# Optimization experiments

Measured on AMD Instinct MI355X. Metric: run time of the kernel, lower is better.

## Reference

```python
import math
import jax, jax.numpy as jnp
import numpy as np

B, S, D = 1, 2048, 4096
H, KV, Dh = 32, 8, 128          # query heads, kv heads, head dim
G = H // KV                      # GQA group size
THETA = 10000.0
FACTOR = 4.0
BETA_FAST, BETA_SLOW, ORIG_MAX = 32, 1, 32768


def _yarn_rope_cache(seq_len):
    """YaRN-scaled RoPE cos/sin cache, matching YaRNRotaryEmbedding._build_cache."""
    inv_freq = 1.0 / (THETA ** (np.arange(0, Dh, 2, dtype=np.float32) / Dh))
    low = ORIG_MAX / (2 * math.pi * BETA_SLOW)
    high = ORIG_MAX / (2 * math.pi * BETA_FAST)
    freq = 1.0 / inv_freq
    smooth = np.clip((freq - low) / (high - low), 0.0, 1.0)
    inv_freq = (1.0 - smooth) * inv_freq + smooth * (inv_freq / FACTOR)
    t = np.arange(seq_len, dtype=np.float32)
    freqs = np.outer(t, inv_freq)                 # [S, Dh/2]
    emb = np.concatenate([freqs, freqs], axis=-1) # [S, Dh]
    return np.cos(emb).astype(np.float32), np.sin(emb).astype(np.float32)


def _rotate_half(x):
    x1, x2 = jnp.split(x, 2, axis=-1)
    return jnp.concatenate([-x2, x1], axis=-1)


def setup_inputs() -> dict:
    key = jax.random.key(0)
    k0, k1, k2, k3, k4 = jax.random.split(key, 5)
    scale = 0.02
    hidden_states = jax.random.normal(k0, (B, S, D), jnp.float32)
    Wq = jax.random.normal(k1, (H * Dh, D), jnp.float32) * scale
    Wk = jax.random.normal(k2, (KV * Dh, D), jnp.float32) * scale
    Wv = jax.random.normal(k3, (KV * Dh, D), jnp.float32) * scale
    Wo = jax.random.normal(k4, (D, H * Dh), jnp.float32) * scale
    cos_np, sin_np = _yarn_rope_cache(S)
    return {"hidden_states": hidden_states, "Wq": Wq, "Wk": Wk, "Wv": Wv,
            "Wo": Wo, "cos": jnp.asarray(cos_np), "sin": jnp.asarray(sin_np)}


def reference(hidden_states, Wq, Wk, Wv, Wo, cos, sin):
    x = hidden_states
    b, s, _ = x.shape
    # QKV projections (Linear, no bias): y = x @ W.T
    q = jnp.einsum('bsd,ed->bse', x, Wq).reshape(b, s, H, Dh).transpose(0, 2, 1, 3)   # [B,H,S,Dh]
    k = jnp.einsum('bsd,ed->bse', x, Wk).reshape(b, s, KV, Dh).transpose(0, 2, 1, 3)  # [B,KV,S,Dh]
    v = jnp.einsum('bsd,ed->bse', x, Wv).reshape(b, s, KV, Dh).transpose(0, 2, 1, 3)  # [B,KV,S,Dh]
    # YaRN RoPE (cos/sin: [S,Dh], broadcast over batch/head)
    c = cos[None, None, :, :]
    sn = sin[None, None, :, :]
    q = q * c + _rotate_half(q) * sn
    k = k * c + _rotate_half(k) * sn
    # GQA: group query heads over kv heads instead of materializing repeat_interleave
    qg = q.reshape(b, KV, G, s, Dh)
    scores = jnp.einsum('bkgqd,bknd->bkgqn', qg, k) / math.sqrt(Dh)  # [B,KV,G,S,S]
    causal = jnp.tril(jnp.ones((s, s), dtype=bool))
    scores = jnp.where(causal[None, None, None], scores, jnp.finfo(scores.dtype).min)
    w = jax.nn.softmax(scores.astype(jnp.float32), axis=-1).astype(x.dtype)
    attn = jnp.einsum('bkgqn,bknd->bkgqd', w, v)                      # [B,KV,G,S,Dh]
    attn = attn.reshape(b, H, s, Dh).transpose(0, 2, 1, 3).reshape(b, s, H * Dh)
    return jnp.einsum('bse,de->bsd', attn, Wo)
```

## Files before the change

### kernel.cpp

```cpp
#include <hip/hip_runtime.h>

#define S_LEN 2048
#define DMODEL 4096
#define NH 32
#define NKV 8
#define DH 128
#define QDIM (NH*DH)
#define NQKV 6144
#define SCALE 0.08838834764831845f

typedef __attribute__((ext_vector_type(8))) short short8;
typedef __attribute__((ext_vector_type(4))) float f32x4;
typedef __attribute__((ext_vector_type(4))) unsigned short us4;

__device__ __forceinline__ unsigned short f2bf(float f) {
  union { float f; unsigned int u; } v; v.f = f;
  unsigned int r = v.u + 0x7FFFu + ((v.u >> 16) & 1u);
  return (unsigned short)(r >> 16);
}
__device__ __forceinline__ float bf2f(unsigned short h) {
  union { unsigned int u; float f; } v; v.u = ((unsigned int)h) << 16;
  return v.f;
}

__global__ __launch_bounds__(256) void cvt_all(const float* __restrict__ x,
                                               const float* __restrict__ Wq,
                                               const float* __restrict__ Wk,
                                               const float* __restrict__ Wv,
                                               unsigned short* __restrict__ xb,
                                               unsigned short* __restrict__ Wqkvb) {
  const int blk = blockIdx.x;
  const float* src; unsigned short* dst; int off;
  if (blk < 8192)       { src = x;  dst = xb;               off = blk; }
  else if (blk < 24576) { src = Wq; dst = Wqkvb;            off = blk - 8192; }
  else if (blk < 28672) { src = Wk; dst = Wqkvb + 16777216; off = blk - 24576; }
  else                  { src = Wv; dst = Wqkvb + 20971520; off = blk - 28672; }
  int i = off * 256 + threadIdx.x;
  const float4 f = reinterpret_cast<const float4*>(src)[i];
  us4 o;
  o.x = f2bf(f.x); o.y = f2bf(f.y); o.z = f2bf(f.z); o.w = f2bf(f.w);
  reinterpret_cast<us4*>(dst)[i] = o;
}

template<int M_, int N_, int K_, int BM_, int BN_, int OUT_BF16, int CHN>
__global__ __launch_bounds__(512) void gemm8p(const unsigned short* __restrict__ A,
                                              const unsigned short* __restrict__ B,
                                              void* __restrict__ Cv) {
  constexpr int ATILE = BM_ * 128;
  constexpr int BTILE = BN_ * 128;
  constexpr int BUF = ATILE + BTILE;
  constexpr int LPA = BM_ / 64;
  constexpr int LPB = BN_ / 64;
  constexpr int VM  = LPA + LPB;
  constexpr int MI = BM_ / 32, NF = BN_ / 64;
  constexpr int MIL = MI / 2, NFL = NF / 2;
  constexpr int NT = K_ / 64;
  __shared__ char lds[2 * BUF];

  const int tid = threadIdx.x;
  const int lane = tid & 63, wave = tid >> 6;
  const int wm = wave >> 2, wn = wave & 3;
  const int fr = lane & 15, fq = lane >> 4;

  const int lin = blockIdx.x;
  const int xcd = lin & 7;
  const int slot = lin >> 3;
  const long n0 = (long)(xcd * CHN + slot % CHN) * BN_;
  const long m0 = (long)(slot / CHN) * BM_;

  auto STAGE_A = [&](int t, int c) {
#pragma unroll
    for (int u = 0; u < LPA; ++u) {
      int b = u * 8192 + tid * 16;
      int row = b >> 7;
      int off = (b & 127) ^ ((row & 7) << 4);
      __builtin_amdgcn_global_load_lds(
        (const __attribute__((address_space(1))) void*)((const char*)A + ((m0 + row) * (long)K_ + t * 64) * 2 + off),
        (__attribute__((address_space(3))) void*)(lds + c * BUF + b), 16, 0, 0);
    }
  };
  auto STAGE_B = [&](int t, int c) {
#pragma unroll
    for (int u = 0; u < LPB; ++u) {
      int b = u * 8192 + tid * 16;
      int row = b >> 7;
      int off = (b & 127) ^ ((row & 7) << 4);
      __builtin_amdgcn_global_load_lds(
        (const __attribute__((address_space(1))) void*)((const char*)B + ((n0 + row) * (long)K_ + t * 64) * 2 + off),
        (__attribute__((address_space(3))) void*)(lds + c * BUF + ATILE + b), 16, 0, 0);
    }
  };
#define VMCNT_STEADY() do { if constexpr (VM == 6) asm volatile("s_waitcnt vmcnt(6)" ::: "memory"); \
                            else if constexpr (VM == 7) asm volatile("s_waitcnt vmcnt(7)" ::: "memory"); \
                            else asm volatile("s_waitcnt vmcnt(8)" ::: "memory"); } while (0)

  f32x4 acc[MI][NF] = {};
  short8 af[MI][2];
  short8 bf[NF][2];

  STAGE_A(0, 0); STAGE_B(0, 0);
  STAGE_A(1, 1); STAGE_B(1, 1);
  VMCNT_STEADY();
  __builtin_amdgcn_s_barrier();

  for (int t = 0; t < NT; ++t) {
    const int c = t & 1;
    const char* tb = lds + c * BUF;

#pragma unroll
    for (int mi = 0; mi < MIL; ++mi) {
      int row = wm * (BM_ / 2) + mi * 16 + fr;
#pragma unroll
      for (int ks = 0; ks < 2; ++ks)
        af[mi][ks] = *(const short8*)(tb + row * 128 + ((ks * 64 + fq * 16) ^ ((row & 7) << 4)));
    }
#pragma unroll
    for (int ni = 0; ni < NFL; ++ni) {
      int row = wn * (BN_ / 4) + ni * 16 + fr;
#pragma unroll
      for (int ks = 0; ks < 2; ++ks)
        bf[ni][ks] = *(const short8*)(tb + ATILE + row * 128 + ((ks * 64 + fq * 16) ^ ((row & 7) << 4)));
    }
    __builtin_amdgcn_s_barrier();
    __builtin_amdgcn_s_setprio(1);
#pragma unroll
    for (int mi = 0; mi < MIL; ++mi)
#pragma unroll
      for (int ni = 0; ni < NFL; ++ni)
#pragma unroll
        for (int ks = 0; ks < 2; ++ks)
          acc[mi][ni] = __builtin_amdgcn_mfma_f32_16x16x32_bf16(af[mi][ks], bf[ni][ks], acc[mi][ni], 0, 0, 0);
    __builtin_amdgcn_s_setprio(0);
    __builtin_amdgcn_s_barrier();

#pragma unroll
    for (int mi = MIL; mi < MI; ++mi) {
      int row = wm * (BM_ / 2) + mi * 16 + fr;
#pragma unroll
      for (int ks = 0; ks < 2; ++ks)
        af[mi][ks] = *(const short8*)(tb + row * 128 + ((ks * 64 + fq * 16) ^ ((row & 7) << 4)));
    }
#pragma unroll
    for (int ni = NFL; ni < NF; ++ni) {
      int row = wn * (BN_ / 4) + ni * 16 + fr;
#pragma unroll
      for (int ks = 0; ks < 2; ++ks)
        bf[ni][ks] = *(const short8*)(tb + ATILE + row * 128 + ((ks * 64 + fq * 16) ^ ((row & 7) << 4)));
    }
    __builtin_amdgcn_s_barrier();
    __builtin_amdgcn_s_setprio(1);
#pragma unroll
    for (int mi = 0; mi < MIL; ++mi)
#pragma unroll
      for (int ni = NFL; ni < NF; ++ni)
#pragma unroll
        for (int ks = 0; ks < 2; ++ks)
          acc[mi][ni] = __builtin_amdgcn_mfma_f32_16x16x32_bf16(af[mi][ks], bf[ni][ks], acc[mi][ni], 0, 0, 0);
    __builtin_amdgcn_s_setprio(0);
    __builtin_amdgcn_s_barrier();

    if (t + 2 < NT) STAGE_A(t + 2, c);
    __builtin_amdgcn_s_setprio(1);
#pragma unroll
    for (int mi = MIL; mi < MI; ++mi)
#pragma unroll
      for (int ni = 0; ni < NFL; ++ni)
#pragma unroll
        for (int ks = 0; ks < 2; ++ks)
          acc[mi][ni] = __builtin_amdgcn_mfma_f32_16x16x32_bf16(af[mi][ks], bf[ni][ks], acc[mi][ni], 0, 0, 0);
    __builtin_amdgcn_s_setprio(0);
    __builtin_amdgcn_s_barrier();

    if (t + 2 < NT) STAGE_B(t + 2, c);
    __builtin_amdgcn_s_setprio(1);
#pragma unroll
    for (int mi = MIL; mi < MI; ++mi)
#pragma unroll
      for (int ni = NFL; ni < NF; ++ni)
#pragma unroll
        for (int ks = 0; ks < 2; ++ks)
          acc[mi][ni] = __builtin_amdgcn_mfma_f32_16x16x32_bf16(af[mi][ks], bf[ni][ks], acc[mi][ni], 0, 0, 0);
    __builtin_amdgcn_s_setprio(0);
    if (t + 2 < NT) { VMCNT_STEADY(); }
    else if (t + 1 < NT) { asm volatile("s_waitcnt vmcnt(0)" ::: "memory"); }
    __builtin_amdgcn_s_barrier();
  }
#undef VMCNT_STEADY

#pragma unroll
  for (int mi = 0; mi < MI; ++mi)
#pragma unroll
    for (int ni = 0; ni < NF; ++ni)
#pragma unroll
      for (int j = 0; j < 4; ++j) {
        long r = m0 + wm * (BM_ / 2) + mi * 16 + fq * 4 + j;
        long cc = n0 + wn * (BN_ / 4) + ni * 16 + fr;
        float v = acc[mi][ni][j];
        if (OUT_BF16) ((unsigned short*)Cv)[r * N_ + cc] = f2bf(v);
        else          ((float*)Cv)[r * N_ + cc] = v;
      }
}

template<int M_, int N_, int K_, int BM_, int BN_, int OUT_BF16, int CHN>
__global__ __launch_bounds__(512) void gemm8p3(const unsigned short* __restrict__ A,
                                               const unsigned short* __restrict__ B,
                                               void* __restrict__ Cv) {
  constexpr int ATILE = BM_ * 128;
  constexpr int BTILE = BN_ * 128;
  constexpr int BUF = ATILE + BTILE;
  constexpr int LPA = BM_ / 64;
  constexpr int LPB = BN_ / 64;
  constexpr int MI = BM_ / 32, NF = BN_ / 64;
  constexpr int MIL = MI / 2, NFL = NF / 2;
  constexpr int NT = K_ / 64;
  __shared__ char lds[3 * BUF];

  const int tid = threadIdx.x;
  const int lane = tid & 63, wave = tid >> 6;
  const int wm = wave >> 2, wn = wave & 3;
  const int fr = lane & 15, fq = lane >> 4;

  const int lin = blockIdx.x;
  const int xcd = lin & 7;
  const int slot = lin >> 3;
  const long n0 = (long)(xcd * CHN + slot % CHN) * BN_;
  const long m0 = (long)(slot / CHN) * BM_;

  auto STAGE_A = [&](int t, int c) {
#pragma unroll
    for (int u = 0; u < LPA; ++u) {
      int b = u * 8192 + tid * 16;
      int row = b >> 7;
      int off = (b & 127) ^ ((row & 7) << 4);
      __builtin_amdgcn_global_load_lds(
        (const __attribute__((address_space(1))) void*)((const char*)A + ((m0 + row) * (long)K_ + t * 64) * 2 + off),
        (__attribute__((address_space(3))) void*)(lds + c * BUF + b), 16, 0, 0);
    }
  };
  auto STAGE_B_HALF = [&](int t, int c, int half) {
#pragma unroll
    for (int u = 0; u < LPB / 2; ++u) {
      int b = (half * (LPB / 2) + u) * 8192 + tid * 16;
      int row = b >> 7;
      int off = (b & 127) ^ ((row & 7) << 4);
      __builtin_amdgcn_global_load_lds(
        (const __attribute__((address_space(1))) void*)((const char*)B + ((n0 + row) * (long)K_ + t * 64) * 2 + off),
        (__attribute__((address_space(3))) void*)(lds + c * BUF + ATILE + b), 16, 0, 0);
    }
  };

  f32x4 acc[MI][NF] = {};
  short8 af[MI][2];
  short8 bf[NF][2];

  STAGE_A(0, 0); STAGE_B_HALF(0, 0, 0); STAGE_B_HALF(0, 0, 1);
  STAGE_A(1, 1); STAGE_B_HALF(1, 1, 0); STAGE_B_HALF(1, 1, 1);
  asm volatile("s_waitcnt vmcnt(0)" ::: "memory");
  __builtin_amdgcn_s_barrier();

  for (int t = 0; t < NT; ++t) {
    const char* tb = lds + (t % 3) * BUF;
    const int c2 = (t + 2) % 3;

#pragma unroll
    for (int mi = 0; mi < MIL; ++mi) {
      int row = wm * (BM_ / 2) + mi * 16 + fr;
#pragma unroll
      for (int ks = 0; ks < 2; ++ks)
        af[mi][ks] = *(const short8*)(tb + row * 128 + ((ks * 64 + fq * 16) ^ ((row & 7) << 4)));
    }
#pragma unroll
    for (int ni = 0; ni < NFL; ++ni) {
      int row = wn * (BN_ / 4) + ni * 16 + fr;
#pragma unroll
      for (int ks = 0; ks < 2; ++ks)
        bf[ni][ks] = *(const short8*)(tb + ATILE + row * 128 + ((ks * 64 + fq * 16) ^ ((row & 7) << 4)));
    }
    if (t + 2 < NT) STAGE_A(t + 2, c2);
    __builtin_amdgcn_s_barrier();
    __builtin_amdgcn_s_setprio(1);
#pragma unroll
    for (int mi = 0; mi < MIL; ++mi)
#pragma unroll
      for (int ni = 0; ni < NFL; ++ni)
#pragma unroll
        for (int ks = 0; ks < 2; ++ks)
          acc[mi][ni] = __builtin_amdgcn_mfma_f32_16x16x32_bf16(af[mi][ks], bf[ni][ks], acc[mi][ni], 0, 0, 0);
    __builtin_amdgcn_s_setprio(0);
    __builtin_amdgcn_s_barrier();

#pragma unroll
    for (int mi = MIL; mi < MI; ++mi) {
      int row = wm * (BM_ / 2) + mi * 16 + fr;
#pragma unroll
      for (int ks = 0; ks < 2; ++ks)
        af[mi][ks] = *(const short8*)(tb + row * 128 + ((ks * 64 + fq * 16) ^ ((row & 7) << 4)));
    }
#pragma unroll
    for (int ni = NFL; ni < NF; ++ni) {
      int row = wn * (BN_ / 4) + ni * 16 + fr;
#pragma unroll
      for (int ks = 0; ks < 2; ++ks)
        bf[ni][ks] = *(const short8*)(tb + ATILE + row * 128 + ((ks * 64 + fq * 16) ^ ((row & 7) << 4)));
    }
    if (t + 2 < NT) STAGE_B_HALF(t + 2, c2, 0);
    __builtin_amdgcn_s_barrier();
    __builtin_amdgcn_s_setprio(1);
#pragma unroll
    for (int mi = 0; mi < MIL; ++mi)
#pragma unroll
      for (int ni = NFL; ni < NF; ++ni)
#pragma unroll
        for (int ks = 0; ks < 2; ++ks)
          acc[mi][ni] = __builtin_amdgcn_mfma_f32_16x16x32_bf16(af[mi][ks], bf[ni][ks], acc[mi][ni], 0, 0, 0);
    __builtin_amdgcn_s_setprio(0);
    __builtin_amdgcn_s_barrier();

    if (t + 2 < NT) STAGE_B_HALF(t + 2, c2, 1);
    __builtin_amdgcn_s_setprio(1);
#pragma unroll
    for (int mi = MIL; mi < MI; ++mi)
#pragma unroll
      for (int ni = 0; ni < NFL; ++ni)
#pragma unroll
        for (int ks = 0; ks < 2; ++ks)
          acc[mi][ni] = __builtin_amdgcn_mfma_f32_16x16x32_bf16(af[mi][ks], bf[ni][ks], acc[mi][ni], 0, 0, 0);
    __builtin_amdgcn_s_setprio(0);
    __builtin_amdgcn_s_barrier();

    __builtin_amdgcn_s_setprio(1);
#pragma unroll
    for (int mi = MIL; mi < MI; ++mi)
#pragma unroll
      for (int ni = NFL; ni < NF; ++ni)
#pragma unroll
        for (int ks = 0; ks < 2; ++ks)
          acc[mi][ni] = __builtin_amdgcn_mfma_f32_16x16x32_bf16(af[mi][ks], bf[ni][ks], acc[mi][ni], 0, 0, 0);
    __builtin_amdgcn_s_setprio(0);
    if (t + 2 < NT) { asm volatile("s_waitcnt vmcnt(6)" ::: "memory"); }
    else if (t + 1 < NT) { asm volatile("s_waitcnt vmcnt(0)" ::: "memory"); }
    __builtin_amdgcn_s_barrier();
  }

#pragma unroll
  for (int mi = 0; mi < MI; ++mi)
#pragma unroll
    for (int ni = 0; ni < NF; ++ni)
#pragma unroll
      for (int j = 0; j < 4; ++j) {
        long r = m0 + wm * (BM_ / 2) + mi * 16 + fq * 4 + j;
        long cc = n0 + wn * (BN_ / 4) + ni * 16 + fr;
        float v = acc[mi][ni][j];
        if (OUT_BF16) ((unsigned short*)Cv)[r * N_ + cc] = f2bf(v);
        else          ((float*)Cv)[r * N_ + cc] = v;
      }
}

__global__ __launch_bounds__(256) void ropek_tv(unsigned short* __restrict__ C,
                                                const float* __restrict__ cosb,
                                                const float* __restrict__ sinb,
                                                unsigned short* __restrict__ VT) {
  __shared__ unsigned short tbuf[64][72];
  const int blk = blockIdx.x;
  if (blk < 4096) {
    int idx = blk * 256 + threadIdx.x;
    int i = idx & 63;
    int t = idx >> 6;
    int hh = t & 7;
    int s = t >> 3;
    unsigned short* row = C + (size_t)s * NQKV + 4096 + hh * DH;
    float c  = cosb[s * DH + i];
    float sn = sinb[s * DH + i];
    float x1 = bf2f(row[i]);
    float x2 = bf2f(row[i + 64]);
    row[i]      = f2bf(x1 * c - x2 * sn);
    row[i + 64] = f2bf(x2 * c + x1 * sn);
    return;
  }
  const int b2 = blk - 4096;
  const unsigned short* Vbuf = C + 5120;
  const int s0 = (b2 & 31) * 64, e0 = (b2 >> 5) * 64;
  const int r = threadIdx.x >> 3, c = (threadIdx.x & 7) * 8;
#pragma unroll
  for (int half = 0; half < 2; ++half) {
    int row = r + half * 32;
    *reinterpret_cast<short8*>(&tbuf[row][c]) =
        *reinterpret_cast<const short8*>(Vbuf + (size_t)(s0 + row) * NQKV + e0 + c);
  }
  __syncthreads();
  const int hh = e0 >> 7, dbase = e0 & 127;
#pragma unroll
  for (int half = 0; half < 2; ++half) {
    int row = r + half * 32;
    short8 o;
#pragma unroll
    for (int j = 0; j < 8; ++j) ((unsigned short*)&o)[j] = tbuf[c + j][row];
    *reinterpret_cast<short8*>(VT + (size_t)hh * (DH * (size_t)S_LEN)
                               + (size_t)(dbase + row) * S_LEN + s0 + c) = o;
  }
}

__global__ __launch_bounds__(256) void attn_fwd(const unsigned short* __restrict__ C,
                                                const unsigned short* __restrict__ VT,
                                                unsigned short* __restrict__ Ob,
                                                const float* __restrict__ Wo,
                                                unsigned short* __restrict__ Wob,
                                                const float* __restrict__ cosb,
                                                const float* __restrict__ sinb) {
  __shared__ unsigned short KVs[2][8192];
  __shared__ unsigned short Pl[4][16 * 40];
  const int tid = threadIdx.x, lane = tid & 63, wave = tid >> 6;
  const int kvh = blockIdx.x & 7;
  const int p = blockIdx.x >> 3;
  const int h = kvh * 4 + wave;
  const int fr = lane & 15, fq = lane >> 4;
  const int q0s[2] = { p * 16, (127 - p) * 16 };
  const int tilesA = (p * 16 + 47) >> 5;
  const int tilesB = ((127 - p) * 16 + 47) >> 5;

  const unsigned short* Qbase = C + (size_t)h * DH;
  const unsigned short* Kbase = C + 4096 + (size_t)kvh * DH;
  const unsigned short* Vbase = VT + (size_t)kvh * (DH * (size_t)S_LEN);

  const int wq0 = blockIdx.x * 8192 + tid;
  float4 wreg;

  short8 qf[2][4];
#pragma unroll
  for (int s = 0; s < 2; ++s)
#pragma unroll
    for (int dc = 0; dc < 4; ++dc)
      qf[s][dc] = *reinterpret_cast<const short8*>(
          Qbase + (size_t)(q0s[s] + fr) * NQKV + dc * 32 + fq * 8);

#pragma unroll
  for (int s = 0; s < 2; ++s) {
    const int row = q0s[s] + fr;
#pragma unroll
    for (int dc = 0; dc < 2; ++dc)
#pragma unroll
      for (int e = 0; e < 8; ++e) {
        int d = dc * 32 + fq * 8 + e;
        float cs = cosb[row * DH + d];
        float sn = sinb[row * DH + d];
        float x1 = bf2f((unsigned short)qf[s][dc][e]);
        float x2 = bf2f((unsigned short)qf[s][dc + 2][e]);
        qf[s][dc][e]     = (short)f2bf((x1 * cs - x2 * sn) * SCALE);
        qf[s][dc + 2][e] = (short)f2bf((x2 * cs + x1 * sn) * SCALE);
      }
  }

  f32x4 o_acc[2][8] = {};
  float mrow[2][4] = {{-1e30f,-1e30f,-1e30f,-1e30f},{-1e30f,-1e30f,-1e30f,-1e30f}};
  float lpart[2][4] = {};

  auto STAGE = [&](int t, int buf) {
    const int kv0 = t * 32;
    char* dst = (char*)&KVs[buf][0];
#pragma unroll
    for (int sh = 0; sh < 2; ++sh) {
      int b = sh * 4096 + tid * 16;
      int krow = b >> 8;
      int kcol = (b & 255) ^ ((krow & 7) << 4);
      __builtin_amdgcn_global_load_lds(
          (const __attribute__((address_space(1))) void*)(Kbase + (size_t)(kv0 + krow) * NQKV + (kcol >> 1)),
          (__attribute__((address_space(3))) void*)(dst + b), 16, 0, 0);
      int vrow = b >> 6;
      int vcol = (b & 63) ^ ((((vrow ^ (vrow >> 2)) & 3)) << 4);
      __builtin_amdgcn_global_load_lds(
          (const __attribute__((address_space(1))) void*)(Vbase + (size_t)vrow * S_LEN + kv0 + (vcol >> 1)),
          (__attribute__((address_space(3))) void*)(dst + 8192 + b), 16, 0, 0);
    }
  };

  int cur = 0;
  STAGE(0, 0);
  asm volatile("s_waitcnt vmcnt(0)" ::: "memory");
  __syncthreads();

  for (int t = 0; t < tilesB; ++t) {
    const int kv0 = t * 32;

    if (t > 0 && t <= 32) {
      us4 o;
      o.x = f2bf(wreg.x); o.y = f2bf(wreg.y); o.z = f2bf(wreg.z); o.w = f2bf(wreg.w);
      reinterpret_cast<us4*>(Wob)[wq0 + (t - 1) * 256] = o;
    }
    if (t < 32) wreg = reinterpret_cast<const float4*>(Wo)[wq0 + t * 256];

    if (t + 1 < tilesB) STAGE(t + 1, cur ^ 1);
    const char* kvb = (const char*)&KVs[cur][0];

#pragma unroll
    for (int s = 0; s < 2; ++s) {
      if (s == 0 && t >= tilesA) continue;
      const int q0 = q0s[s];

      f32x4 sacc[2] = {};
#pragma unroll
      for (int nt = 0; nt < 2; ++nt) {
        const int row = nt * 16 + fr;
#pragma unroll
        for (int dc = 0; dc < 4; ++dc) {
          short8 kf = *reinterpret_cast<const short8*>(
              kvb + row * 256 + ((dc * 64 + fq * 16) ^ ((row & 7) << 4)));
          sacc[nt] = __builtin_amdgcn_mfma_f32_16x16x32_bf16(qf[s][dc], kf, sacc[nt], 0, 0, 0);
        }
      }

      const bool needMask = (kv0 + 32 > q0);
      if (needMask) {
#pragma unroll
        for (int j = 0; j < 4; ++j) {
          int qrow = q0 + fq * 4 + j;
#pragma unroll
          for (int nt = 0; nt < 2; ++nt)
            sacc[nt][j] = ((kv0 + nt*16 + fr) <= qrow) ? sacc[nt][j] : -1e30f;
        }
      }
      bool ok = true;
      float lm[4];
#pragma unroll
      for (int j = 0; j < 4; ++j) {
        lm[j] = fmaxf(sacc[0][j], sacc[1][j]);
        ok = ok && (lm[j] <= mrow[s][j] + 8.f);
      }
      if (!__all(ok)) {
#pragma unroll
        for (int j = 0; j < 4; ++j) {
          float rm = lm[j];
          rm = fmaxf(rm, __shfl_xor(rm, 1));
          rm = fmaxf(rm, __shfl_xor(rm, 2));
          rm = fmaxf(rm, __shfl_xor(rm, 4));
          rm = fmaxf(rm, __shfl_xor(rm, 8));
          float mnew = fmaxf(mrow[s][j], rm);
          float corr = __expf(mrow[s][j] - mnew);
          mrow[s][j] = mnew;
          lpart[s][j] *= corr;
#pragma unroll
          for (int dt = 0; dt < 8; ++dt) o_acc[s][dt][j] *= corr;
        }
      }
#pragma unroll
      for (int j = 0; j < 4; ++j) {
        float p0 = __expf(sacc[0][j] - mrow[s][j]);
        float p1 = __expf(sacc[1][j] - mrow[s][j]);
        lpart[s][j] += p0 + p1;
        unsigned int u;
        asm("v_cvt_pk_bf16_f32 %0, %1, %2" : "=v"(u) : "v"(p0), "v"(p1));
        Pl[wave][(fq*4 + j)*40 + fr]      = (unsigned short)u;
        Pl[wave][(fq*4 + j)*40 + 16 + fr] = (unsigned short)(u >> 16);
      }
      asm volatile("s_waitcnt lgkmcnt(0)" ::: "memory");
      __builtin_amdgcn_sched_barrier(0);

      short8 pa = *reinterpret_cast<const short8*>(&Pl[wave][fr*40 + fq*8]);
#pragma unroll
      for (int dt = 0; dt < 8; ++dt) {
        const int row = dt * 16 + fr;
        short8 bv = *reinterpret_cast<const short8*>(
            kvb + 8192 + row * 64 + ((fq * 16) ^ ((((row ^ (row >> 2)) & 3)) << 4)));
        o_acc[s][dt] = __builtin_amdgcn_mfma_f32_16x16x32_bf16(pa, bv, o_acc[s][dt], 0, 0, 0);
      }
    }

    asm volatile("s_waitcnt vmcnt(0)" ::: "memory");
    __syncthreads();
    cur ^= 1;
  }

#pragma unroll
  for (int s = 0; s < 2; ++s)
#pragma unroll
    for (int j = 0; j < 4; ++j) {
      float l = lpart[s][j];
      l += __shfl_xor(l, 1);
      l += __shfl_xor(l, 2);
      l += __shfl_xor(l, 4);
      l += __shfl_xor(l, 8);
      float inv = 1.f / l;
      size_t r = (size_t)q0s[s] + fq*4 + j;
#pragma unroll
      for (int dt = 0; dt < 8; ++dt)
        Ob[r * QDIM + h * DH + dt*16 + fr] = f2bf(o_acc[s][dt][j] * inv);
    }
}

extern "C" void kernel_launch(void* const* d_in, const int* in_sizes, int n_in,
                              void* d_out, int out_size, void* d_ws, size_t ws_size,
                              hipStream_t stream) {
  (void)in_sizes; (void)n_in; (void)out_size; (void)ws_size;
  const float* x    = (const float*)d_in[0];
  const float* Wq   = (const float*)d_in[1];
  const float* Wk   = (const float*)d_in[2];
  const float* Wv   = (const float*)d_in[3];
  const float* Wo   = (const float*)d_in[4];
  const float* cosb = (const float*)d_in[5];
  const float* sinb = (const float*)d_in[6];

  char* ws = (char*)d_ws;
  unsigned short* xb    = (unsigned short*)(ws);
  unsigned short* Wqkvb = (unsigned short*)(ws + 16777216);
  unsigned short* Wob   = (unsigned short*)(ws + 67108864);
  unsigned short* Cqkv  = (unsigned short*)(ws + 100663296);
  unsigned short* VT    = (unsigned short*)(ws + 125829120);
  unsigned short* Ab    = xb;

  cvt_all<<<32768, 256, 0, stream>>>(x, Wq, Wk, Wv, xb, Wqkvb);

  gemm8p<2048, 6144, 4096, 256, 192, 1, 4><<<256, 512, 0, stream>>>(xb, Wqkvb, Cqkv);

  ropek_tv<<<4608, 256, 0, stream>>>(Cqkv, cosb, sinb, VT);

  attn_fwd<<<512, 256, 0, stream>>>(Cqkv, VT, Ab, Wo, Wob, cosb, sinb);

  gemm8p3<2048, 4096, 4096, 128, 256, 0, 2><<<256, 512, 0, stream>>>(Ab, Wob, d_out);
}
```

Baseline: 288.3 us.

## Fuse fp32-to-bf16 weight conversion into QKV GEMM B-operand loading

Drops the separate conversion pass over Wq/Wk/Wv and has the QKV GEMM read fp32 weights directly, packing them to bf16 in registers before writing them to LDS. This removes a full write and re-read of the 48MB bf16 weight copy. The cost is doubled global bytes on the B operand inside the GEMM and a register round trip instead of direct-to-LDS loads, which may expose latency. The output projection also moves from the triple-buffered GEMM variant back to the double-buffered one.

```diff
diff --git a/kernel.cpp b/kernel.cpp
--- a/kernel.cpp
+++ b/kernel.cpp
@@ -22,24 +22,206 @@
   union { unsigned int u; float f; } v; v.u = ((unsigned int)h) << 16;
   return v.f;
 }
-
-__global__ __launch_bounds__(256) void cvt_all(const float* __restrict__ x,
-                                               const float* __restrict__ Wq,
-                                               const float* __restrict__ Wk,
-                                               const float* __restrict__ Wv,
-                                               unsigned short* __restrict__ xb,
-                                               unsigned short* __restrict__ Wqkvb) {
-  const int blk = blockIdx.x;
-  const float* src; unsigned short* dst; int off;
-  if (blk < 8192)       { src = x;  dst = xb;               off = blk; }
-  else if (blk < 24576) { src = Wq; dst = Wqkvb;            off = blk - 8192; }
-  else if (blk < 28672) { src = Wk; dst = Wqkvb + 16777216; off = blk - 24576; }
-  else                  { src = Wv; dst = Wqkvb + 20971520; off = blk - 28672; }
-  int i = off * 256 + threadIdx.x;
-  const float4 f = reinterpret_cast<const float4*>(src)[i];
+__device__ __forceinline__ short8 pack_bf16x8(float4 a, float4 b) {
+  unsigned int u0, u1, u2, u3;
+  asm("v_cvt_pk_bf16_f32 %0, %1, %2" : "=v"(u0) : "v"(a.x), "v"(a.y));
+  asm("v_cvt_pk_bf16_f32 %0, %1, %2" : "=v"(u1) : "v"(a.z), "v"(a.w));
+  asm("v_cvt_pk_bf16_f32 %0, %1, %2" : "=v"(u2) : "v"(b.x), "v"(b.y));
+  asm("v_cvt_pk_bf16_f32 %0, %1, %2" : "=v"(u3) : "v"(b.z), "v"(b.w));
+  union { unsigned int u[4]; short8 s; } r;
+  r.u[0] = u0; r.u[1] = u1; r.u[2] = u2; r.u[3] = u3;
+  return r.s;
+}
+
+__global__ __launch_bounds__(256) void cvt_x(const float* __restrict__ in,
+                                             unsigned short* __restrict__ out) {
+  int i = blockIdx.x * 256 + threadIdx.x;
+  const float4 f = reinterpret_cast<const float4*>(in)[i];
   us4 o;
   o.x = f2bf(f.x); o.y = f2bf(f.y); o.z = f2bf(f.z); o.w = f2bf(f.w);
-  reinterpret_cast<us4*>(dst)[i] = o;
+  reinterpret_cast<us4*>(out)[i] = o;
+}
+
+__global__ __launch_bounds__(512) void gemm8pqkv(const unsigned short* __restrict__ A,
+                                                 const float* __restrict__ Wq,
+                                                 const float* __restrict__ Wk,
+                                                 const float* __restrict__ Wv,
+                                                 unsigned short* __restrict__ Cv) {
+  constexpr int K_ = 4096, N_ = 6144;
+  constexpr int BM_ = 256, BN_ = 192;
+  constexpr int ATILE = BM_ * 128;
+  constexpr int BTILE = BN_ * 128;
+  constexpr int BUF = ATILE + BTILE;
+  constexpr int LPA = BM_ / 64;
+  constexpr int LPB = BN_ / 64;
+  constexpr int MI = 8, NF = 3;
+  constexpr int MIL = 4, NFL = 1;
+  constexpr int NT = K_ / 64;
+  constexpr int CHN = 4;
+  __shared__ char lds[2 * BUF];
+
+  const int tid = threadIdx.x;
+  const int lane = tid & 63, wave = tid >> 6;
+  const int wm = wave >> 2, wn = wave & 3;
+  const int fr = lane & 15, fq = lane >> 4;
+
+  const int lin = blockIdx.x;
+  const int xcd = lin & 7;
+  const int slot = lin >> 3;
+  const long n0 = (long)(xcd * CHN + slot % CHN) * BN_;
+  const long m0 = (long)(slot / CHN) * BM_;
+
+  const char* pB[LPB];
+  int bslot[LPB];
+#pragma unroll
+  for (int u = 0; u < LPB; ++u) {
+    int b = u * 8192 + tid * 16;
+    int row = b >> 7;
+    int colx = (b & 127) ^ ((row & 7) << 4);
+    long n = n0 + row;
+    const float* base = (n < 4096) ? Wq + n * (long)K_
+                      : (n < 5120) ? Wk + (n - 4096) * (long)K_
+                                   : Wv + (n - 5120) * (long)K_;
+    pB[u] = (const char*)base + (long)colx * 2;
+    bslot[u] = b;
+  }
+  float4 breg[LPB][2];
+
+  auto B_ISSUE = [&](int t) {
+#pragma unroll
+    for (int u = 0; u < LPB; ++u) {
+      breg[u][0] = *reinterpret_cast<const float4*>(pB[u] + (long)t * 256);
+      breg[u][1] = *reinterpret_cast<const float4*>(pB[u] + (long)t * 256 + 16);
+    }
+  };
+  auto B_WRITE = [&](int c) {
+#pragma unroll
+    for (int u = 0; u < LPB; ++u)
+      *reinterpret_cast<short8*>(lds + c * BUF + ATILE + bslot[u]) =
+          pack_bf16x8(breg[u][0], breg[u][1]);
+  };
+  auto STAGE_A = [&](int t, int c) {
+#pragma unroll
+    for (int u = 0; u < LPA; ++u) {
+      int b = u * 8192 + tid * 16;
+      int row = b >> 7;
+      int off = (b & 127) ^ ((row & 7) << 4);
+      __builtin_amdgcn_global_load_lds(
+        (const __attribute__((address_space(1))) void*)((const char*)A + ((m0 + row) * (long)K_ + t * 64) * 2 + off),
+        (__attribute__((address_space(3))) void*)(lds + c * BUF + b), 16, 0, 0);
+    }
+  };
+
+  f32x4 acc[MI][NF] = {};
+  short8 af[MI][2];
+  short8 bf[NF][2];
+
+  B_ISSUE(0);
+  asm volatile("s_waitcnt vmcnt(0)" ::: "memory");
+  B_WRITE(0);
+  B_ISSUE(1);
+  STAGE_A(0, 0); STAGE_A(1, 1);
+  asm volatile("s_waitcnt vmcnt(8)" ::: "memory");
+  B_WRITE(1);
+  asm volatile("s_waitcnt vmcnt(0)" ::: "memory");
+  asm volatile("s_waitcnt lgkmcnt(0)" ::: "memory");
+  __builtin_amdgcn_s_barrier();
+
+  for (int t = 0; t < NT; ++t) {
+    const int c = t & 1;
+    const char* tb = lds + c * BUF;
+
+#pragma unroll
+    for (int mi = 0; mi < MIL; ++mi) {
+      int row = wm * (BM_ / 2) + mi * 16 + fr;
+#pragma unroll
+      for (int ks = 0; ks < 2; ++ks)
+        af[mi][ks] = *(const short8*)(tb + row * 128 + ((ks * 64 + fq * 16) ^ ((row & 7) << 4)));
+    }
+#pragma unroll
+    for (int ni = 0; ni < NFL; ++ni) {
+      int row = wn * (BN_ / 4) + ni * 16 + fr;
+#pragma unroll
+      for (int ks = 0; ks < 2; ++ks)
+        bf[ni][ks] = *(const short8*)(tb + ATILE + row * 128 + ((ks * 64 + fq * 16) ^ ((row & 7) << 4)));
+    }
+    asm volatile("s_waitcnt vmcnt(4)" ::: "memory");
+    if (t > 0 && t + 1 < NT) B_WRITE((t + 1) & 1);
+    if (t + 2 < NT) B_ISSUE(t + 2);
+    __builtin_amdgcn_s_barrier();
+    __builtin_amdgcn_s_setprio(1);
+#pragma unroll
+    for (int mi = 0; mi < MIL; ++mi)
+#pragma unroll
+      for (int ni = 0; ni < NFL; ++ni)
+#pragma unroll
+        for (int ks = 0; ks < 2; ++ks)
+          acc[mi][ni] = __builtin_amdgcn_mfma_f32_16x16x32_bf16(af[mi][ks], bf[ni][ks], acc[mi][ni], 0, 0, 0);
+    __builtin_amdgcn_s_setprio(0);
+    __builtin_amdgcn_s_barrier();
+
+#pragma unroll
+    for (int mi = MIL; mi < MI; ++mi) {
+      int row = wm * (BM_ / 2) + mi * 16 + fr;
+#pragma unroll
+      for (int ks = 0; ks < 2; ++ks)
+        af[mi][ks] = *(const short8*)(tb + row * 128 + ((ks * 64 + fq * 16) ^ ((row & 7) << 4)));
+    }
+#pragma unroll
+    for (int ni = NFL; ni < NF; ++ni) {
+      int row = wn * (BN_ / 4) + ni * 16 + fr;
+#pragma unroll
+      for (int ks = 0; ks < 2; ++ks)
+        bf[ni][ks] = *(const short8*)(tb + ATILE + row * 128 + ((ks * 64 + fq * 16) ^ ((row & 7) << 4)));
+    }
+    __builtin_amdgcn_s_barrier();
+    __builtin_amdgcn_s_setprio(1);
+#pragma unroll
+    for (int mi = 0; mi < MIL; ++mi)
+#pragma unroll
+      for (int ni = NFL; ni < NF; ++ni)
+#pragma unroll
+        for (int ks = 0; ks < 2; ++ks)
+          acc[mi][ni] = __builtin_amdgcn_mfma_f32_16x16x32_bf16(af[mi][ks], bf[ni][ks], acc[mi][ni], 0, 0, 0);
+    __builtin_amdgcn_s_setprio(0);
+    __builtin_amdgcn_s_barrier();
+
+    if (t + 2 < NT) STAGE_A(t + 2, c);
+    __builtin_amdgcn_s_setprio(1);
+#pragma unroll
+    for (int mi = MIL; mi < MI; ++mi)
+#pragma unroll
+      for (int ni = 0; ni < NFL; ++ni)
+#pragma unroll
+        for (int ks = 0; ks < 2; ++ks)
+          acc[mi][ni] = __builtin_amdgcn_mfma_f32_16x16x32_bf16(af[mi][ks], bf[ni][ks], acc[mi][ni], 0, 0, 0);
+    __builtin_amdgcn_s_setprio(0);
+    __builtin_amdgcn_s_barrier();
+
+    __builtin_amdgcn_s_setprio(1);
+#pragma unroll
+    for (int mi = MIL; mi < MI; ++mi)
+#pragma unroll
+      for (int ni = NFL; ni < NF; ++ni)
+#pragma unroll
+        for (int ks = 0; ks < 2; ++ks)
+          acc[mi][ni] = __builtin_amdgcn_mfma_f32_16x16x32_bf16(af[mi][ks], bf[ni][ks], acc[mi][ni], 0, 0, 0);
+    __builtin_amdgcn_s_setprio(0);
+    if (t + 2 < NT) { asm volatile("s_waitcnt vmcnt(10)" ::: "memory"); }
+    else if (t + 1 < NT) { asm volatile("s_waitcnt vmcnt(0)" ::: "memory"); }
+    __builtin_amdgcn_s_barrier();
+  }
+
+#pragma unroll
+  for (int mi = 0; mi < MI; ++mi)
+#pragma unroll
+    for (int ni = 0; ni < NF; ++ni)
+#pragma unroll
+      for (int j = 0; j < 4; ++j) {
+        long r = m0 + wm * (BM_ / 2) + mi * 16 + fq * 4 + j;
+        long cc = n0 + wn * (BN_ / 4) + ni * 16 + fr;
+        Cv[r * N_ + cc] = f2bf(acc[mi][ni][j]);
+      }
 }
 
 template<int M_, int N_, int K_, int BM_, int BN_, int OUT_BF16, int CHN>
@@ -186,161 +368,6 @@
     __builtin_amdgcn_s_barrier();
   }
 #undef VMCNT_STEADY
-
-#pragma unroll
-  for (int mi = 0; mi < MI; ++mi)
-#pragma unroll
-    for (int ni = 0; ni < NF; ++ni)
-#pragma unroll
-      for (int j = 0; j < 4; ++j) {
-        long r = m0 + wm * (BM_ / 2) + mi * 16 + fq * 4 + j;
-        long cc = n0 + wn * (BN_ / 4) + ni * 16 + fr;
-        float v = acc[mi][ni][j];
-        if (OUT_BF16) ((unsigned short*)Cv)[r * N_ + cc] = f2bf(v);
-        else          ((float*)Cv)[r * N_ + cc] = v;
-      }
-}
-
-template<int M_, int N_, int K_, int BM_, int BN_, int OUT_BF16, int CHN>
-__global__ __launch_bounds__(512) void gemm8p3(const unsigned short* __restrict__ A,
-                                               const unsigned short* __restrict__ B,
-                                               void* __restrict__ Cv) {
-  constexpr int ATILE = BM_ * 128;
-  constexpr int BTILE = BN_ * 128;
-  constexpr int BUF = ATILE + BTILE;
-  constexpr int LPA = BM_ / 64;
-  constexpr int LPB = BN_ / 64;
-  constexpr int MI = BM_ / 32, NF = BN_ / 64;
-  constexpr int MIL = MI / 2, NFL = NF / 2;
-  constexpr int NT = K_ / 64;
-  __shared__ char lds[3 * BUF];
-
-  const int tid = threadIdx.x;
-  const int lane = tid & 63, wave = tid >> 6;
-  const int wm = wave >> 2, wn = wave & 3;
-  const int fr = lane & 15, fq = lane >> 4;
-
-  const int lin = blockIdx.x;
-  const int xcd = lin & 7;
-  const int slot = lin >> 3;
-  const long n0 = (long)(xcd * CHN + slot % CHN) * BN_;
-  const long m0 = (long)(slot / CHN) * BM_;
-
-  auto STAGE_A = [&](int t, int c) {
-#pragma unroll
-    for (int u = 0; u < LPA; ++u) {
-      int b = u * 8192 + tid * 16;
-      int row = b >> 7;
-      int off = (b & 127) ^ ((row & 7) << 4);
-      __builtin_amdgcn_global_load_lds(
-        (const __attribute__((address_space(1))) void*)((const char*)A + ((m0 + row) * (long)K_ + t * 64) * 2 + off),
-        (__attribute__((address_space(3))) void*)(lds + c * BUF + b), 16, 0, 0);
-    }
-  };
-  auto STAGE_B_HALF = [&](int t, int c, int half) {
-#pragma unroll
-    for (int u = 0; u < LPB / 2; ++u) {
-      int b = (half * (LPB / 2) + u) * 8192 + tid * 16;
-      int row = b >> 7;
-      int off = (b & 127) ^ ((row & 7) << 4);
-      __builtin_amdgcn_global_load_lds(
-        (const __attribute__((address_space(1))) void*)((const char*)B + ((n0 + row) * (long)K_ + t * 64) * 2 + off),
-        (__attribute__((address_space(3))) void*)(lds + c * BUF + ATILE + b), 16, 0, 0);
-    }
-  };
-
-  f32x4 acc[MI][NF] = {};
-  short8 af[MI][2];
-  short8 bf[NF][2];
-
-  STAGE_A(0, 0); STAGE_B_HALF(0, 0, 0); STAGE_B_HALF(0, 0, 1);
-  STAGE_A(1, 1); STAGE_B_HALF(1, 1, 0); STAGE_B_HALF(1, 1, 1);
-  asm volatile("s_waitcnt vmcnt(0)" ::: "memory");
-  __builtin_amdgcn_s_barrier();
-
-  for (int t = 0; t < NT; ++t) {
-    const char* tb = lds + (t % 3) * BUF;
-    const int c2 = (t + 2) % 3;
-
-#pragma unroll
-    for (int mi = 0; mi < MIL; ++mi) {
-      int row = wm * (BM_ / 2) + mi * 16 + fr;
-#pragma unroll
-      for (int ks = 0; ks < 2; ++ks)
-        af[mi][ks] = *(const short8*)(tb + row * 128 + ((ks * 64 + fq * 16) ^ ((row & 7) << 4)));
-    }
-#pragma unroll
-    for (int ni = 0; ni < NFL; ++ni) {
-      int row = wn * (BN_ / 4) + ni * 16 + fr;
-#pragma unroll
-      for (int ks = 0; ks < 2; ++ks)
-        bf[ni][ks] = *(const short8*)(tb + ATILE + row * 128 + ((ks * 64 + fq * 16) ^ ((row & 7) << 4)));
-    }
-    if (t + 2 < NT) STAGE_A(t + 2, c2);
-    __builtin_amdgcn_s_barrier();
-    __builtin_amdgcn_s_setprio(1);
-#pragma unroll
-    for (int mi = 0; mi < MIL; ++mi)
-#pragma unroll
-      for (int ni = 0; ni < NFL; ++ni)
-#pragma unroll
-        for (int ks = 0; ks < 2; ++ks)
-          acc[mi][ni] = __builtin_amdgcn_mfma_f32_16x16x32_bf16(af[mi][ks], bf[ni][ks], acc[mi][ni], 0, 0, 0);
-    __builtin_amdgcn_s_setprio(0);
-    __builtin_amdgcn_s_barrier();
-
-#pragma unroll
-    for (int mi = MIL; mi < MI; ++mi) {
-      int row = wm * (BM_ / 2) + mi * 16 + fr;
-#pragma unroll
-      for (int ks = 0; ks < 2; ++ks)
-        af[mi][ks] = *(const short8*)(tb + row * 128 + ((ks * 64 + fq * 16) ^ ((row & 7) << 4)));
-    }
-#pragma unroll
-    for (int ni = NFL; ni < NF; ++ni) {
-      int row = wn * (BN_ / 4) + ni * 16 + fr;
-#pragma unroll
-      for (int ks = 0; ks < 2; ++ks)
-        bf[ni][ks] = *(const short8*)(tb + ATILE + row * 128 + ((ks * 64 + fq * 16) ^ ((row & 7) << 4)));
-    }
-    if (t + 2 < NT) STAGE_B_HALF(t + 2, c2, 0);
-    __builtin_amdgcn_s_barrier();
-    __builtin_amdgcn_s_setprio(1);
-#pragma unroll
-    for (int mi = 0; mi < MIL; ++mi)
-#pragma unroll
-      for (int ni = NFL; ni < NF; ++ni)
-#pragma unroll
-        for (int ks = 0; ks < 2; ++ks)
-          acc[mi][ni] = __builtin_amdgcn_mfma_f32_16x16x32_bf16(af[mi][ks], bf[ni][ks], acc[mi][ni], 0, 0, 0);
-    __builtin_amdgcn_s_setprio(0);
-    __builtin_amdgcn_s_barrier();
-
-    if (t + 2 < NT) STAGE_B_HALF(t + 2, c2, 1);
-    __builtin_amdgcn_s_setprio(1);
-#pragma unroll
-    for (int mi = MIL; mi < MI; ++mi)
-#pragma unroll
-      for (int ni = 0; ni < NFL; ++ni)
-#pragma unroll
-        for (int ks = 0; ks < 2; ++ks)
-          acc[mi][ni] = __builtin_amdgcn_mfma_f32_16x16x32_bf16(af[mi][ks], bf[ni][ks], acc[mi][ni], 0, 0, 0);
-    __builtin_amdgcn_s_setprio(0);
-    __builtin_amdgcn_s_barrier();
-
-    __builtin_amdgcn_s_setprio(1);
-#pragma unroll
-    for (int mi = MIL; mi < MI; ++mi)
-#pragma unroll
-      for (int ni = NFL; ni < NF; ++ni)
-#pragma unroll
-        for (int ks = 0; ks < 2; ++ks)
-          acc[mi][ni] = __builtin_amdgcn_mfma_f32_16x16x32_bf16(af[mi][ks], bf[ni][ks], acc[mi][ni], 0, 0, 0);
-    __builtin_amdgcn_s_setprio(0);
-    if (t + 2 < NT) { asm volatile("s_waitcnt vmcnt(6)" ::: "memory"); }
-    else if (t + 1 < NT) { asm volatile("s_waitcnt vmcnt(0)" ::: "memory"); }
-    __builtin_amdgcn_s_barrier();
-  }
 
 #pragma unroll
   for (int mi = 0; mi < MI; ++mi)
@@ -600,19 +627,18 @@
 
   char* ws = (char*)d_ws;
   unsigned short* xb    = (unsigned short*)(ws);
-  unsigned short* Wqkvb = (unsigned short*)(ws + 16777216);
   unsigned short* Wob   = (unsigned short*)(ws + 67108864);
   unsigned short* Cqkv  = (unsigned short*)(ws + 100663296);
   unsigned short* VT    = (unsigned short*)(ws + 125829120);
   unsigned short* Ab    = xb;
 
-  cvt_all<<<32768, 256, 0, stream>>>(x, Wq, Wk, Wv, xb, Wqkvb);
-
-  gemm8p<2048, 6144, 4096, 256, 192, 1, 4><<<256, 512, 0, stream>>>(xb, Wqkvb, Cqkv);
+  cvt_x<<<8192, 256, 0, stream>>>(x, xb);
+
+  gemm8pqkv<<<256, 512, 0, stream>>>(xb, Wq, Wk, Wv, Cqkv);
 
   ropek_tv<<<4608, 256, 0, stream>>>(Cqkv, cosb, sinb, VT);
 
   attn_fwd<<<512, 256, 0, stream>>>(Cqkv, VT, Ab, Wo, Wob, cosb, sinb);
 
-  gemm8p3<2048, 4096, 4096, 128, 256, 0, 2><<<256, 512, 0, stream>>>(Ab, Wob, d_out);
-}
+  gemm8p<2048, 4096, 4096, 128, 256, 0, 2><<<256, 512, 0, stream>>>(Ab, Wob, d_out);
+}
```

After: 285.3 us (median of 3 runs). No clear change (-1.0%).
